# Kernel tuning notes

Hardware: AMD Instinct MI355X
Metric: run time of the kernel (lower is better)

## Reference

```python
import jax, jax.numpy as jnp
import numpy as np

N_NODES = 50000
N_EDGES = 1000000
IN_F = 128
OUT_F = 32
HEADS = 4


def setup_inputs() -> dict:
    key = jax.random.key(0)
    k1, k2, k3, k4, k5 = jax.random.split(key, 5)
    x = jax.random.normal(k1, (N_NODES, IN_F), dtype=jnp.float32)
    edge_index = jax.random.randint(k2, (2, N_EDGES), 0, N_NODES, dtype=jnp.int64)
    # nn.Linear weight: [out_features*heads, in_features], xavier_uniform
    lim_W = float(np.sqrt(6.0 / (IN_F + OUT_F * HEADS)))
    W = jax.random.uniform(k3, (OUT_F * HEADS, IN_F), dtype=jnp.float32, minval=-lim_W, maxval=lim_W)
    lim_a = float(np.sqrt(6.0 / (HEADS + OUT_F)))  # xavier on [1, heads, out]
    a_src = jax.random.uniform(k4, (1, HEADS, OUT_F), dtype=jnp.float32, minval=-lim_a, maxval=lim_a)
    a_dst = jax.random.uniform(k5, (1, HEADS, OUT_F), dtype=jnp.float32, minval=-lim_a, maxval=lim_a)
    return {"x": x, "edge_index": edge_index, "W": W, "a_src": a_src, "a_dst": a_dst}


def reference(x, edge_index, W, a_src, a_dst):
    N = x.shape[0]
    h, f = HEADS, OUT_F
    # Linear (no bias) then split heads: [N, h, f]
    x_trans = (x @ W.T).reshape(N, h, f)
    src, dst = edge_index[0], edge_index[1]
    x_src = x_trans[src]                      # [E, h, f] edge gather
    x_dst = x_trans[dst]                      # [E, h, f]
    attn_src = jnp.einsum('ehf,ohf->eh', x_src, a_src)  # a_* have leading 1 broadcast dim
    attn_dst = jnp.einsum('ehf,ohf->eh', x_dst, a_dst)
    scores = jax.nn.leaky_relu(attn_src + attn_dst, negative_slope=0.2)  # [E, h]
    # Faithful to original: softmax over dim=0 (ALL edges globally per head)
    attn_w = jax.nn.softmax(scores, axis=0)   # [E, h]; dropout = identity (eval)
    weighted = x_src * attn_w[:, :, None]     # [E, h, f]
    out = jax.ops.segment_sum(weighted, dst, num_segments=N)  # scatter-add over dst
    return out.reshape(N, h * f)
```

## Files before the change

### kernel.cpp

```cpp
#include <hip/hip_runtime.h>

#define HEADS 4
#define BKSH 5
#define CAP 896
#define MAXBK 1600

typedef short bf16x8 __attribute__((ext_vector_type(8)));
typedef float f32x4  __attribute__((ext_vector_type(4)));

__device__ __forceinline__ unsigned short f2bf(float f) {
    unsigned u = __float_as_uint(f);
    return (unsigned short)((u + 0x7FFFu + ((u >> 16) & 1u)) >> 16);
}
__device__ __forceinline__ int detect64(const int* __restrict__ ei32) {
    unsigned long long b = __ballot(ei32[2 * (threadIdx.x & 63) + 1] != 0);
    return (b == 0ULL) ? 1 : 0;
}
__device__ __forceinline__ void load_edge(const void* ei, int is64, long E, long e,
                                          long* s, long* d) {
    if (is64) {
        *s = (long)((const long long*)ei)[e];
        *d = (long)((const long long*)ei)[E + e];
    } else {
        *s = (long)((const int*)ei)[e];
        *d = (long)((const int*)ei)[E + e];
    }
}

__launch_bounds__(256)
__global__ void k_prep(const float* __restrict__ W, const float* __restrict__ avs,
                       const float* __restrict__ avd, unsigned short* __restrict__ Wb,
                       float* __restrict__ gs, float* __restrict__ gd,
                       int* __restrict__ cursor, float* __restrict__ sums, int nbk) {
    const int b = blockIdx.x, t = threadIdx.x;
    if (b < 16) {
        const int i = (b * 256 + t) * 4;
        const float4 v = *(const float4*)(W + i);
        ushort4 u;
        u.x = f2bf(v.x); u.y = f2bf(v.y); u.z = f2bf(v.z); u.w = f2bf(v.w);
        *(ushort4*)(Wb + i) = u;
    } else if (b == 16) {
        const int h = t >> 6, k0 = (t & 63) * 2;
        float s0 = 0.f, s1 = 0.f, d0 = 0.f, d1 = 0.f;
        for (int o = 0; o < 32; ++o) {
            const float as = avs[h * 32 + o], ad = avd[h * 32 + o];
            const float w0 = W[(h * 32 + o) * 128 + k0];
            const float w1 = W[(h * 32 + o) * 128 + k0 + 1];
            s0 = fmaf(as, w0, s0); s1 = fmaf(as, w1, s1);
            d0 = fmaf(ad, w0, d0); d1 = fmaf(ad, w1, d1);
        }
        gs[h * 128 + k0] = s0; gs[h * 128 + k0 + 1] = s1;
        gd[h * 128 + k0] = d0; gd[h * 128 + k0 + 1] = d1;
    } else {
        for (int i = t; i < nbk; i += 256) cursor[i] = 0;
        if (t < 4) sums[t] = 0.f;
    }
}

__launch_bounds__(256)
__global__ void k_mfma_scores(const float* __restrict__ x, const unsigned short* __restrict__ Wb,
                              const float* __restrict__ gs, const float* __restrict__ gd,
                              unsigned short* __restrict__ xt, float* __restrict__ ss,
                              float* __restrict__ sd, int N, int NG) {
    if ((int)blockIdx.x >= NG) {
        const int lane = threadIdx.x & 63;
        const int wid = __builtin_amdgcn_readfirstlane(threadIdx.x >> 6);
        const int n = ((int)blockIdx.x - NG) * 64 + lane;
        if (n >= N) return;
        const float4* __restrict__ xr  = (const float4*)(x + (long)n * 128);
        const float4* __restrict__ gsr = (const float4*)(gs + wid * 128);
        const float4* __restrict__ gdr = (const float4*)(gd + wid * 128);
        float vs = 0.f, vd = 0.f;
#pragma unroll
        for (int j = 0; j < 32; ++j) {
            const float4 xv = xr[j];
            const float4 gv = gsr[j];
            const float4 dv = gdr[j];
            vs = fmaf(xv.x, gv.x, fmaf(xv.y, gv.y, fmaf(xv.z, gv.z, fmaf(xv.w, gv.w, vs))));
            vd = fmaf(xv.x, dv.x, fmaf(xv.y, dv.y, fmaf(xv.z, dv.z, fmaf(xv.w, dv.w, vd))));
        }
        ss[n * 4 + wid] = vs;
        sd[n * 4 + wid] = vd;
        return;
    }
    const int lane = threadIdx.x & 63;
    const int wid = threadIdx.x >> 6;
    const int c = lane & 15, g = lane >> 4;
    const int m0 = blockIdx.x * 64 + wid * 16;
    const long row = (long)((m0 + c) < N ? (m0 + c) : (N - 1));
    const float4* __restrict__ xr = (const float4*)(x + row * 128);

    bf16x8 A[4];
#pragma unroll
    for (int ks = 0; ks < 4; ++ks) {
        const float4 f0 = xr[ks * 8 + g * 2];
        const float4 f1 = xr[ks * 8 + g * 2 + 1];
        bf16x8 a;
        a[0] = (short)f2bf(f0.x); a[1] = (short)f2bf(f0.y);
        a[2] = (short)f2bf(f0.z); a[3] = (short)f2bf(f0.w);
        a[4] = (short)f2bf(f1.x); a[5] = (short)f2bf(f1.y);
        a[6] = (short)f2bf(f1.z); a[7] = (short)f2bf(f1.w);
        A[ks] = a;
    }
#pragma unroll
    for (int to = 0; to < 8; ++to) {
        f32x4 acc = {0.f, 0.f, 0.f, 0.f};
#pragma unroll
        for (int ks = 0; ks < 4; ++ks) {
            const bf16x8 bv = *(const bf16x8*)(Wb + (long)(to * 16 + c) * 128 + ks * 32 + g * 8);
            acc = __builtin_amdgcn_mfma_f32_16x16x32_bf16(A[ks], bv, acc, 0, 0, 0);
        }
#pragma unroll
        for (int j = 0; j < 4; ++j) {
            const int n = m0 + g * 4 + j;
            if (n < N) xt[(long)n * 128 + to * 16 + c] = f2bf(acc[j]);
        }
    }
}

__launch_bounds__(1024)
__global__ void k_part(const void* __restrict__ ei, const float* __restrict__ ss,
                       const float* __restrict__ sd, int* __restrict__ cursor,
                       unsigned* __restrict__ ebuf, float* __restrict__ sums,
                       long E, int nbk) {
    __shared__ int hist[MAXBK];
    __shared__ int base[MAXBK];
    __shared__ float sm[16][4];
    const int t = threadIdx.x;
    const int is64 = detect64((const int*)ei);
    for (int i = t; i < nbk; i += 1024) hist[i] = 0;
    __syncthreads();

    const long e0 = (long)blockIdx.x * 4096;
    int sreg[4], dreg[4], rreg[4];
    float w0 = 0.f, w1 = 0.f, w2 = 0.f, w3 = 0.f;
#pragma unroll
    for (int j = 0; j < 4; ++j) {
        const long e = e0 + (long)j * 1024 + t;
        sreg[j] = -1;
        if (e < E) {
            long s, d;
            load_edge(ei, is64, E, e, &s, &d);
            sreg[j] = (int)s; dreg[j] = (int)d;
            rreg[j] = atomicAdd(&hist[(int)d >> BKSH], 1);
            const float4 a = ((const float4*)ss)[s];
            const float4 b = ((const float4*)sd)[d];
            float sc;
            sc = a.x + b.x; sc = sc > 0.f ? sc : 0.2f * sc; w0 += __expf(sc);
            sc = a.y + b.y; sc = sc > 0.f ? sc : 0.2f * sc; w1 += __expf(sc);
            sc = a.z + b.z; sc = sc > 0.f ? sc : 0.2f * sc; w2 += __expf(sc);
            sc = a.w + b.w; sc = sc > 0.f ? sc : 0.2f * sc; w3 += __expf(sc);
        }
    }
    __syncthreads();
    for (int i = t; i < nbk; i += 1024)
        base[i] = hist[i] ? atomicAdd(&cursor[i], hist[i]) : 0;
    __syncthreads();
#pragma unroll
    for (int j = 0; j < 4; ++j) {
        if (sreg[j] >= 0) {
            const int b = dreg[j] >> BKSH;
            const int pos = base[b] + rreg[j];
            if (pos < CAP)
                ebuf[(long)b * CAP + pos] =
                    ((unsigned)(dreg[j] & 31) << 16) | (unsigned)sreg[j];
        }
    }
#pragma unroll
    for (int m = 32; m; m >>= 1) {
        w0 += __shfl_xor(w0, m);
        w1 += __shfl_xor(w1, m);
        w2 += __shfl_xor(w2, m);
        w3 += __shfl_xor(w3, m);
    }
    const int wvi = t >> 6;
    if ((t & 63) == 0) { sm[wvi][0] = w0; sm[wvi][1] = w1; sm[wvi][2] = w2; sm[wvi][3] = w3; }
    __syncthreads();
    if (t < 4) {
        float v = 0.f;
#pragma unroll
        for (int i = 0; i < 16; ++i) v += sm[i][t];
        atomicAdd(&sums[t], v);
    }
}

__launch_bounds__(256)
__global__ void k_bgather(const unsigned* __restrict__ ebuf, const int* __restrict__ cursor,
                          const float* __restrict__ ss, const float* __restrict__ sd,
                          const float* __restrict__ sums, const unsigned* __restrict__ xt16,
                          float* __restrict__ out, int N) {
    __shared__ int cnt[32];
    __shared__ int row[33];
    __shared__ int cur[32];
    __shared__ unsigned lsrc[CAP];
    __shared__ float4 lwt[CAP];
    const int t = threadIdx.x;
    const int b = blockIdx.x;
    const int n0 = b << BKSH;
    if (t < 32) cnt[t] = 0;
    __syncthreads();
    const int c0v = cursor[b];
    const int m = c0v < CAP ? c0v : CAP;
    const unsigned* __restrict__ seg = ebuf + (long)b * CAP;
    for (int i = t; i < m; i += 256) atomicAdd(&cnt[seg[i] >> 16], 1);
    __syncthreads();
    if (t < 32) {
        const int v = cnt[t];
        int incl = v;
#pragma unroll
        for (int s = 1; s < 32; s <<= 1) {
            const int u = __shfl_up(incl, s);
            if (t >= s) incl += u;
        }
        row[t] = incl - v;
        cur[t] = incl - v;
        if (t == 31) row[32] = incl;
    }
    __syncthreads();
    for (int i = t; i < m; i += 256) {
        const unsigned u = seg[i];
        const int s = (int)(u & 0xFFFFu), dl = (int)(u >> 16);
        const int pos = atomicAdd(&cur[dl], 1);
        lsrc[pos] = (unsigned)s;
        const float4 a = ((const float4*)ss)[s];
        const float4 bb = ((const float4*)sd)[n0 + dl];
        float4 w; float sc;
        sc = a.x + bb.x; sc = sc > 0.f ? sc : 0.2f * sc; w.x = __expf(sc);
        sc = a.y + bb.y; sc = sc > 0.f ? sc : 0.2f * sc; w.y = __expf(sc);
        sc = a.z + bb.z; sc = sc > 0.f ? sc : 0.2f * sc; w.z = __expf(sc);
        sc = a.w + bb.w; sc = sc > 0.f ? sc : 0.2f * sc; w.w = __expf(sc);
        lwt[pos] = w;
    }
    __syncthreads();

    const int wv = t >> 6, l = t & 63, h = l >> 4;
    const float* __restrict__ lwtf = (const float*)lwt;
    const float invh = 1.0f / sums[h];
    for (int d8 = 0; d8 < 8; ++d8) {
        const int dl = wv * 8 + d8;
        const int n = n0 + dl;
        if (n >= N) break;
        const int beg = row[dl], end = row[dl + 1];
        float ax = 0.f, ay = 0.f;
        int i = beg;
        for (; i + 4 <= end; i += 4) {
            const int s0 = (int)lsrc[i + 0];
            const int s1 = (int)lsrc[i + 1];
            const int s2 = (int)lsrc[i + 2];
            const int s3 = (int)lsrc[i + 3];
            const float w0 = lwtf[(i + 0) * 4 + h];
            const float w1 = lwtf[(i + 1) * 4 + h];
            const float w2 = lwtf[(i + 2) * 4 + h];
            const float w3 = lwtf[(i + 3) * 4 + h];
            const unsigned x0 = xt16[(long)s0 * 64 + l];
            const unsigned x1 = xt16[(long)s1 * 64 + l];
            const unsigned x2 = xt16[(long)s2 * 64 + l];
            const unsigned x3 = xt16[(long)s3 * 64 + l];
            ax = fmaf(w0, __uint_as_float(x0 << 16), ax);
            ay = fmaf(w0, __uint_as_float(x0 & 0xFFFF0000u), ay);
            ax = fmaf(w1, __uint_as_float(x1 << 16), ax);
            ay = fmaf(w1, __uint_as_float(x1 & 0xFFFF0000u), ay);
            ax = fmaf(w2, __uint_as_float(x2 << 16), ax);
            ay = fmaf(w2, __uint_as_float(x2 & 0xFFFF0000u), ay);
            ax = fmaf(w3, __uint_as_float(x3 << 16), ax);
            ay = fmaf(w3, __uint_as_float(x3 & 0xFFFF0000u), ay);
        }
        for (; i < end; ++i) {
            const int s = (int)lsrc[i];
            const float wt = lwtf[i * 4 + h];
            const unsigned xv = xt16[(long)s * 64 + l];
            ax = fmaf(wt, __uint_as_float(xv << 16), ax);
            ay = fmaf(wt, __uint_as_float(xv & 0xFFFF0000u), ay);
        }
        ((float2*)out)[(long)n * 64 + l] = make_float2(ax * invh, ay * invh);
    }
}

extern "C" void kernel_launch(void* const* d_in, const int* in_sizes, int n_in,
                              void* d_out, int out_size, void* d_ws, size_t ws_size,
                              hipStream_t stream) {
    const float* x     = (const float*)d_in[0];
    const void*  ei    = d_in[1];
    const float* W     = (const float*)d_in[2];
    const float* a_src = (const float*)d_in[3];
    const float* a_dst = (const float*)d_in[4];
    const long N = in_sizes[0] / 128;
    const long E = in_sizes[1] / 2;
    const int NG  = (int)((N + 63) / 64);
    const int nbk = (int)((N + 31) / 32);
    const int NP  = (int)((E + 4095) / 4096);

    char* p = (char*)d_ws;
    auto alloc = [&](size_t bytes) { char* r = p; p += (bytes + 15) & ~(size_t)15; return r; };
    unsigned*       xt16   = (unsigned*)alloc(N * 64 * 4);
    float*          ss     = (float*)alloc(N * 4 * 4);
    float*          sd     = (float*)alloc(N * 4 * 4);
    unsigned*       ebuf   = (unsigned*)alloc((size_t)nbk * CAP * 4);
    int*            cursor = (int*)alloc(nbk * 4);
    float*          sums   = (float*)alloc(4 * 4);
    unsigned short* Wb     = (unsigned short*)alloc(128 * 128 * 2);
    float*          gs     = (float*)alloc(4 * 128 * 4);
    float*          gd     = (float*)alloc(4 * 128 * 4);

    float* out = (float*)d_out;

    k_prep<<<18, 256, 0, stream>>>(W, a_src, a_dst, Wb, gs, gd, cursor, sums, nbk);
    k_mfma_scores<<<(unsigned)(2 * NG), 256, 0, stream>>>(x, Wb, gs, gd,
                                                          (unsigned short*)xt16,
                                                          ss, sd, (int)N, NG);
    k_part<<<(unsigned)NP, 1024, 0, stream>>>(ei, ss, sd, cursor, ebuf, sums, E, nbk);
    k_bgather<<<(unsigned)nbk, 256, 0, stream>>>(ebuf, cursor, ss, sd, sums, xt16,
                                                 out, (int)N);
}
```

Baseline: 105.1 us.

## Fuse attention score projection into MFMA linear kernel; unroll gather by eight

The src/dst score dot products (x·gs, x·gd) move into the MFMA transform kernel. They reuse the x rows each lane already loads for the bf16 A fragments, with partial sums reduced across the four lane groups by shuffles. This drops the separate half of the grid that re-read all of x in fp32, halving x traffic in that stage. The gather loop in k_bgather is also unrolled from 4 to 8 edges so more independent loads are in flight, at some cost in register pressure.

```diff
diff --git a/kernel.cpp b/kernel.cpp
--- a/kernel.cpp
+++ b/kernel.cpp
@@ -58,39 +58,29 @@
 }
 
 __launch_bounds__(256)
-__global__ void k_mfma_scores(const float* __restrict__ x, const unsigned short* __restrict__ Wb,
-                              const float* __restrict__ gs, const float* __restrict__ gd,
-                              unsigned short* __restrict__ xt, float* __restrict__ ss,
-                              float* __restrict__ sd, int N, int NG) {
-    if ((int)blockIdx.x >= NG) {
-        const int lane = threadIdx.x & 63;
-        const int wid = __builtin_amdgcn_readfirstlane(threadIdx.x >> 6);
-        const int n = ((int)blockIdx.x - NG) * 64 + lane;
-        if (n >= N) return;
-        const float4* __restrict__ xr  = (const float4*)(x + (long)n * 128);
-        const float4* __restrict__ gsr = (const float4*)(gs + wid * 128);
-        const float4* __restrict__ gdr = (const float4*)(gd + wid * 128);
-        float vs = 0.f, vd = 0.f;
-#pragma unroll
-        for (int j = 0; j < 32; ++j) {
-            const float4 xv = xr[j];
-            const float4 gv = gsr[j];
-            const float4 dv = gdr[j];
-            vs = fmaf(xv.x, gv.x, fmaf(xv.y, gv.y, fmaf(xv.z, gv.z, fmaf(xv.w, gv.w, vs))));
-            vd = fmaf(xv.x, dv.x, fmaf(xv.y, dv.y, fmaf(xv.z, dv.z, fmaf(xv.w, dv.w, vd))));
-        }
-        ss[n * 4 + wid] = vs;
-        sd[n * 4 + wid] = vd;
-        return;
-    }
-    const int lane = threadIdx.x & 63;
-    const int wid = threadIdx.x >> 6;
+__global__ void k_mfma(const float* __restrict__ x, const unsigned short* __restrict__ Wb,
+                       const float* __restrict__ gs, const float* __restrict__ gd,
+                       unsigned short* __restrict__ xt, float* __restrict__ ss,
+                       float* __restrict__ sd, int N) {
+    __shared__ float gsl[512], gdl[512];
+    const int t = threadIdx.x;
+    if (t < 128) {
+        ((float4*)gsl)[t] = ((const float4*)gs)[t];
+        ((float4*)gdl)[t] = ((const float4*)gd)[t];
+    }
+    __syncthreads();
+
+    const int lane = t & 63;
+    const int wid = t >> 6;
     const int c = lane & 15, g = lane >> 4;
     const int m0 = blockIdx.x * 64 + wid * 16;
-    const long row = (long)((m0 + c) < N ? (m0 + c) : (N - 1));
+    const int nrow = m0 + c;
+    const long row = (long)(nrow < N ? nrow : (N - 1));
     const float4* __restrict__ xr = (const float4*)(x + row * 128);
 
     bf16x8 A[4];
+    float vs0 = 0.f, vs1 = 0.f, vs2 = 0.f, vs3 = 0.f;
+    float vd0 = 0.f, vd1 = 0.f, vd2 = 0.f, vd3 = 0.f;
 #pragma unroll
     for (int ks = 0; ks < 4; ++ks) {
         const float4 f0 = xr[ks * 8 + g * 2];
@@ -101,7 +91,36 @@
         a[4] = (short)f2bf(f1.x); a[5] = (short)f2bf(f1.y);
         a[6] = (short)f2bf(f1.z); a[7] = (short)f2bf(f1.w);
         A[ks] = a;
-    }
+        const int kb = ks * 32 + g * 8;
+#pragma unroll
+        for (int h = 0; h < 4; ++h) {
+            const float4 G0 = *(const float4*)(gsl + h * 128 + kb);
+            const float4 G1 = *(const float4*)(gsl + h * 128 + kb + 4);
+            const float4 D0 = *(const float4*)(gdl + h * 128 + kb);
+            const float4 D1 = *(const float4*)(gdl + h * 128 + kb + 4);
+            float s = fmaf(f0.x, G0.x, fmaf(f0.y, G0.y, fmaf(f0.z, G0.z, f0.w * G0.w)));
+            s = fmaf(f1.x, G1.x, fmaf(f1.y, G1.y, fmaf(f1.z, G1.z, fmaf(f1.w, G1.w, s))));
+            float d = fmaf(f0.x, D0.x, fmaf(f0.y, D0.y, fmaf(f0.z, D0.z, f0.w * D0.w)));
+            d = fmaf(f1.x, D1.x, fmaf(f1.y, D1.y, fmaf(f1.z, D1.z, fmaf(f1.w, D1.w, d))));
+            if (h == 0) { vs0 += s; vd0 += d; }
+            else if (h == 1) { vs1 += s; vd1 += d; }
+            else if (h == 2) { vs2 += s; vd2 += d; }
+            else { vs3 += s; vd3 += d; }
+        }
+    }
+    vs0 += __shfl_xor(vs0, 16); vs0 += __shfl_xor(vs0, 32);
+    vs1 += __shfl_xor(vs1, 16); vs1 += __shfl_xor(vs1, 32);
+    vs2 += __shfl_xor(vs2, 16); vs2 += __shfl_xor(vs2, 32);
+    vs3 += __shfl_xor(vs3, 16); vs3 += __shfl_xor(vs3, 32);
+    vd0 += __shfl_xor(vd0, 16); vd0 += __shfl_xor(vd0, 32);
+    vd1 += __shfl_xor(vd1, 16); vd1 += __shfl_xor(vd1, 32);
+    vd2 += __shfl_xor(vd2, 16); vd2 += __shfl_xor(vd2, 32);
+    vd3 += __shfl_xor(vd3, 16); vd3 += __shfl_xor(vd3, 32);
+    if (g == 0 && nrow < N) {
+        ((float4*)ss)[nrow] = make_float4(vs0, vs1, vs2, vs3);
+        ((float4*)sd)[nrow] = make_float4(vd0, vd1, vd2, vd3);
+    }
+
 #pragma unroll
     for (int to = 0; to < 8; ++to) {
         f32x4 acc = {0.f, 0.f, 0.f, 0.f};
@@ -243,27 +262,19 @@
         const int beg = row[dl], end = row[dl + 1];
         float ax = 0.f, ay = 0.f;
         int i = beg;
-        for (; i + 4 <= end; i += 4) {
-            const int s0 = (int)lsrc[i + 0];
-            const int s1 = (int)lsrc[i + 1];
-            const int s2 = (int)lsrc[i + 2];
-            const int s3 = (int)lsrc[i + 3];
-            const float w0 = lwtf[(i + 0) * 4 + h];
-            const float w1 = lwtf[(i + 1) * 4 + h];
-            const float w2 = lwtf[(i + 2) * 4 + h];
-            const float w3 = lwtf[(i + 3) * 4 + h];
-            const unsigned x0 = xt16[(long)s0 * 64 + l];
-            const unsigned x1 = xt16[(long)s1 * 64 + l];
-            const unsigned x2 = xt16[(long)s2 * 64 + l];
-            const unsigned x3 = xt16[(long)s3 * 64 + l];
-            ax = fmaf(w0, __uint_as_float(x0 << 16), ax);
-            ay = fmaf(w0, __uint_as_float(x0 & 0xFFFF0000u), ay);
-            ax = fmaf(w1, __uint_as_float(x1 << 16), ax);
-            ay = fmaf(w1, __uint_as_float(x1 & 0xFFFF0000u), ay);
-            ax = fmaf(w2, __uint_as_float(x2 << 16), ax);
-            ay = fmaf(w2, __uint_as_float(x2 & 0xFFFF0000u), ay);
-            ax = fmaf(w3, __uint_as_float(x3 << 16), ax);
-            ay = fmaf(w3, __uint_as_float(x3 & 0xFFFF0000u), ay);
+        for (; i + 8 <= end; i += 8) {
+            int sarr[8]; float warr[8]; unsigned xv[8];
+#pragma unroll
+            for (int j = 0; j < 8; ++j) sarr[j] = (int)lsrc[i + j];
+#pragma unroll
+            for (int j = 0; j < 8; ++j) warr[j] = lwtf[(i + j) * 4 + h];
+#pragma unroll
+            for (int j = 0; j < 8; ++j) xv[j] = xt16[(long)sarr[j] * 64 + l];
+#pragma unroll
+            for (int j = 0; j < 8; ++j) {
+                ax = fmaf(warr[j], __uint_as_float(xv[j] << 16), ax);
+                ay = fmaf(warr[j], __uint_as_float(xv[j] & 0xFFFF0000u), ay);
+            }
         }
         for (; i < end; ++i) {
             const int s = (int)lsrc[i];
@@ -304,10 +315,9 @@
 
     float* out = (float*)d_out;
 
-    k_prep<<<18, 256, 0, stream>>>(W, a_src, a_dst, Wb, gs, gd, cursor, sums, nbk);
-    k_mfma_scores<<<(unsigned)(2 * NG), 256, 0, stream>>>(x, Wb, gs, gd,
-                                                          (unsigned short*)xt16,
-                                                          ss, sd, (int)N, NG);
+    k_prep<<<18, 256, 0, stream>>>(W, a_src, a_dst, Wb, gs, gd, cursor, sums, (int)nbk);
+    k_mfma<<<(unsigned)NG, 256, 0, stream>>>(x, Wb, gs, gd, (unsigned short*)xt16,
+                                             ss, sd, (int)N);
     k_part<<<(unsigned)NP, 1024, 0, stream>>>(ei, ss, sd, cursor, ebuf, sums, E, nbk);
     k_bgather<<<(unsigned)nbk, 256, 0, stream>>>(ebuf, cursor, ss, sd, sums, xt16,
                                                  out, (int)N);
```

Measured after the change: 97.74 us. -7.0%, faster.

## Reschedule kernels: fold scores into prep, run MFMA projection alongside edge partition

Applied to the files above, without the earlier changes.

The pipeline is regrouped from four launches into three. The per-node attention-score dot products now run in the prep kernel, with the folded attention vectors recomputed per block into shared memory. The bf16 MFMA projection now shares one launch with the edge partition/histogram pass at 512 threads per block. This removes a launch boundary and lets the GEMM and the edge bucketing overlap on the GPU. The cost is that every score block redundantly recomputes the gs/gd vectors, and the partition blocks change shape (512 threads, 8 edges per thread).

```diff
diff --git a/kernel.cpp b/kernel.cpp
--- a/kernel.cpp
+++ b/kernel.cpp
@@ -28,10 +28,11 @@
 }
 
 __launch_bounds__(256)
-__global__ void k_prep(const float* __restrict__ W, const float* __restrict__ avs,
-                       const float* __restrict__ avd, unsigned short* __restrict__ Wb,
-                       float* __restrict__ gs, float* __restrict__ gd,
-                       int* __restrict__ cursor, float* __restrict__ sums, int nbk) {
+__global__ void k_pre(const float* __restrict__ W, const float* __restrict__ avs,
+                      const float* __restrict__ avd, const float* __restrict__ x,
+                      unsigned short* __restrict__ Wb, float* __restrict__ ss,
+                      float* __restrict__ sd, int* __restrict__ cursor,
+                      float* __restrict__ sums, int nbk, int N) {
     const int b = blockIdx.x, t = threadIdx.x;
     if (b < 16) {
         const int i = (b * 256 + t) * 4;
@@ -39,7 +40,15 @@
         ushort4 u;
         u.x = f2bf(v.x); u.y = f2bf(v.y); u.z = f2bf(v.z); u.w = f2bf(v.w);
         *(ushort4*)(Wb + i) = u;
-    } else if (b == 16) {
+        return;
+    }
+    if (b == 16) {
+        for (int i = t; i < nbk; i += 256) cursor[i] = 0;
+        if (t < 4) sums[t] = 0.f;
+        return;
+    }
+    __shared__ float gsl[512], gdl[512];
+    {
         const int h = t >> 6, k0 = (t & 63) * 2;
         float s0 = 0.f, s1 = 0.f, d0 = 0.f, d1 = 0.f;
         for (int o = 0; o < 32; ++o) {
@@ -49,94 +58,87 @@
             s0 = fmaf(as, w0, s0); s1 = fmaf(as, w1, s1);
             d0 = fmaf(ad, w0, d0); d1 = fmaf(ad, w1, d1);
         }
-        gs[h * 128 + k0] = s0; gs[h * 128 + k0 + 1] = s1;
-        gd[h * 128 + k0] = d0; gd[h * 128 + k0 + 1] = d1;
-    } else {
-        for (int i = t; i < nbk; i += 256) cursor[i] = 0;
-        if (t < 4) sums[t] = 0.f;
-    }
-}
-
-__launch_bounds__(256)
-__global__ void k_mfma_scores(const float* __restrict__ x, const unsigned short* __restrict__ Wb,
-                              const float* __restrict__ gs, const float* __restrict__ gd,
-                              unsigned short* __restrict__ xt, float* __restrict__ ss,
-                              float* __restrict__ sd, int N, int NG) {
-    if ((int)blockIdx.x >= NG) {
-        const int lane = threadIdx.x & 63;
-        const int wid = __builtin_amdgcn_readfirstlane(threadIdx.x >> 6);
-        const int n = ((int)blockIdx.x - NG) * 64 + lane;
-        if (n >= N) return;
-        const float4* __restrict__ xr  = (const float4*)(x + (long)n * 128);
-        const float4* __restrict__ gsr = (const float4*)(gs + wid * 128);
-        const float4* __restrict__ gdr = (const float4*)(gd + wid * 128);
-        float vs = 0.f, vd = 0.f;
-#pragma unroll
-        for (int j = 0; j < 32; ++j) {
-            const float4 xv = xr[j];
-            const float4 gv = gsr[j];
-            const float4 dv = gdr[j];
-            vs = fmaf(xv.x, gv.x, fmaf(xv.y, gv.y, fmaf(xv.z, gv.z, fmaf(xv.w, gv.w, vs))));
-            vd = fmaf(xv.x, dv.x, fmaf(xv.y, dv.y, fmaf(xv.z, dv.z, fmaf(xv.w, dv.w, vd))));
-        }
-        ss[n * 4 + wid] = vs;
-        sd[n * 4 + wid] = vd;
-        return;
-    }
-    const int lane = threadIdx.x & 63;
-    const int wid = threadIdx.x >> 6;
-    const int c = lane & 15, g = lane >> 4;
-    const int m0 = blockIdx.x * 64 + wid * 16;
-    const long row = (long)((m0 + c) < N ? (m0 + c) : (N - 1));
-    const float4* __restrict__ xr = (const float4*)(x + row * 128);
-
-    bf16x8 A[4];
-#pragma unroll
-    for (int ks = 0; ks < 4; ++ks) {
-        const float4 f0 = xr[ks * 8 + g * 2];
-        const float4 f1 = xr[ks * 8 + g * 2 + 1];
-        bf16x8 a;
-        a[0] = (short)f2bf(f0.x); a[1] = (short)f2bf(f0.y);
-        a[2] = (short)f2bf(f0.z); a[3] = (short)f2bf(f0.w);
-        a[4] = (short)f2bf(f1.x); a[5] = (short)f2bf(f1.y);
-        a[6] = (short)f2bf(f1.z); a[7] = (short)f2bf(f1.w);
-        A[ks] = a;
-    }
-#pragma unroll
-    for (int to = 0; to < 8; ++to) {
-        f32x4 acc = {0.f, 0.f, 0.f, 0.f};
-#pragma unroll
-        for (int ks = 0; ks < 4; ++ks) {
-            const bf16x8 bv = *(const bf16x8*)(Wb + (long)(to * 16 + c) * 128 + ks * 32 + g * 8);
-            acc = __builtin_amdgcn_mfma_f32_16x16x32_bf16(A[ks], bv, acc, 0, 0, 0);
-        }
-#pragma unroll
-        for (int j = 0; j < 4; ++j) {
-            const int n = m0 + g * 4 + j;
-            if (n < N) xt[(long)n * 128 + to * 16 + c] = f2bf(acc[j]);
-        }
-    }
-}
-
-__launch_bounds__(1024)
-__global__ void k_part(const void* __restrict__ ei, const float* __restrict__ ss,
-                       const float* __restrict__ sd, int* __restrict__ cursor,
-                       unsigned* __restrict__ ebuf, float* __restrict__ sums,
-                       long E, int nbk) {
+        gsl[h * 128 + k0] = s0; gsl[h * 128 + k0 + 1] = s1;
+        gdl[h * 128 + k0] = d0; gdl[h * 128 + k0 + 1] = d1;
+    }
+    __syncthreads();
+    const int lane = t & 63;
+    const int wid = t >> 6;
+    const int n = (b - 17) * 64 + lane;
+    if (n >= N) return;
+    const float4* __restrict__ xr  = (const float4*)(x + (long)n * 128);
+    const float4* __restrict__ gsr = (const float4*)(gsl + wid * 128);
+    const float4* __restrict__ gdr = (const float4*)(gdl + wid * 128);
+    float vs = 0.f, vd = 0.f;
+#pragma unroll
+    for (int j = 0; j < 32; ++j) {
+        const float4 xv = xr[j];
+        const float4 gv = gsr[j];
+        const float4 dv = gdr[j];
+        vs = fmaf(xv.x, gv.x, fmaf(xv.y, gv.y, fmaf(xv.z, gv.z, fmaf(xv.w, gv.w, vs))));
+        vd = fmaf(xv.x, dv.x, fmaf(xv.y, dv.y, fmaf(xv.z, dv.z, fmaf(xv.w, dv.w, vd))));
+    }
+    ss[n * 4 + wid] = vs;
+    sd[n * 4 + wid] = vd;
+}
+
+__launch_bounds__(512)
+__global__ void k_mp(const float* __restrict__ x, const unsigned short* __restrict__ Wb,
+                     const void* __restrict__ ei, const float* __restrict__ ss,
+                     const float* __restrict__ sd, unsigned short* __restrict__ xt,
+                     int* __restrict__ cursor, unsigned* __restrict__ ebuf,
+                     float* __restrict__ sums, int N, int NG2, long E, int nbk) {
     __shared__ int hist[MAXBK];
     __shared__ int base[MAXBK];
-    __shared__ float sm[16][4];
+    __shared__ float sm[8][4];
     const int t = threadIdx.x;
+    if ((int)blockIdx.x < NG2) {
+        const int lane = t & 63;
+        const int wid = t >> 6;
+        const int c = lane & 15, g = lane >> 4;
+        const int m0 = blockIdx.x * 128 + wid * 16;
+        const int nrow = m0 + c;
+        const long row = (long)(nrow < N ? nrow : (N - 1));
+        const float4* __restrict__ xr = (const float4*)(x + row * 128);
+
+        bf16x8 A[4];
+#pragma unroll
+        for (int ks = 0; ks < 4; ++ks) {
+            const float4 f0 = xr[ks * 8 + g * 2];
+            const float4 f1 = xr[ks * 8 + g * 2 + 1];
+            bf16x8 a;
+            a[0] = (short)f2bf(f0.x); a[1] = (short)f2bf(f0.y);
+            a[2] = (short)f2bf(f0.z); a[3] = (short)f2bf(f0.w);
+            a[4] = (short)f2bf(f1.x); a[5] = (short)f2bf(f1.y);
+            a[6] = (short)f2bf(f1.z); a[7] = (short)f2bf(f1.w);
+            A[ks] = a;
+        }
+#pragma unroll
+        for (int to = 0; to < 8; ++to) {
+            f32x4 acc = {0.f, 0.f, 0.f, 0.f};
+#pragma unroll
+            for (int ks = 0; ks < 4; ++ks) {
+                const bf16x8 bv = *(const bf16x8*)(Wb + (long)(to * 16 + c) * 128 + ks * 32 + g * 8);
+                acc = __builtin_amdgcn_mfma_f32_16x16x32_bf16(A[ks], bv, acc, 0, 0, 0);
+            }
+#pragma unroll
+            for (int j = 0; j < 4; ++j) {
+                const int n = m0 + g * 4 + j;
+                if (n < N) xt[(long)n * 128 + to * 16 + c] = f2bf(acc[j]);
+            }
+        }
+        return;
+    }
     const int is64 = detect64((const int*)ei);
-    for (int i = t; i < nbk; i += 1024) hist[i] = 0;
-    __syncthreads();
-
-    const long e0 = (long)blockIdx.x * 4096;
-    int sreg[4], dreg[4], rreg[4];
+    for (int i = t; i < nbk; i += 512) hist[i] = 0;
+    __syncthreads();
+
+    const long e0 = (long)((int)blockIdx.x - NG2) * 4096;
+    int sreg[8], dreg[8], rreg[8];
     float w0 = 0.f, w1 = 0.f, w2 = 0.f, w3 = 0.f;
 #pragma unroll
-    for (int j = 0; j < 4; ++j) {
-        const long e = e0 + (long)j * 1024 + t;
+    for (int j = 0; j < 8; ++j) {
+        const long e = e0 + (long)j * 512 + t;
         sreg[j] = -1;
         if (e < E) {
             long s, d;
@@ -153,11 +155,11 @@
         }
     }
     __syncthreads();
-    for (int i = t; i < nbk; i += 1024)
+    for (int i = t; i < nbk; i += 512)
         base[i] = hist[i] ? atomicAdd(&cursor[i], hist[i]) : 0;
     __syncthreads();
 #pragma unroll
-    for (int j = 0; j < 4; ++j) {
+    for (int j = 0; j < 8; ++j) {
         if (sreg[j] >= 0) {
             const int b = dreg[j] >> BKSH;
             const int pos = base[b] + rreg[j];
@@ -179,7 +181,7 @@
     if (t < 4) {
         float v = 0.f;
 #pragma unroll
-        for (int i = 0; i < 16; ++i) v += sm[i][t];
+        for (int i = 0; i < 8; ++i) v += sm[i][t];
         atomicAdd(&sums[t], v);
     }
 }
@@ -287,6 +289,7 @@
     const long N = in_sizes[0] / 128;
     const long E = in_sizes[1] / 2;
     const int NG  = (int)((N + 63) / 64);
+    const int NG2 = (int)((N + 127) / 128);
     const int nbk = (int)((N + 31) / 32);
     const int NP  = (int)((E + 4095) / 4096);
 
@@ -299,16 +302,14 @@
     int*            cursor = (int*)alloc(nbk * 4);
     float*          sums   = (float*)alloc(4 * 4);
     unsigned short* Wb     = (unsigned short*)alloc(128 * 128 * 2);
-    float*          gs     = (float*)alloc(4 * 128 * 4);
-    float*          gd     = (float*)alloc(4 * 128 * 4);
 
     float* out = (float*)d_out;
 
-    k_prep<<<18, 256, 0, stream>>>(W, a_src, a_dst, Wb, gs, gd, cursor, sums, nbk);
-    k_mfma_scores<<<(unsigned)(2 * NG), 256, 0, stream>>>(x, Wb, gs, gd,
-                                                          (unsigned short*)xt16,
-                                                          ss, sd, (int)N, NG);
-    k_part<<<(unsigned)NP, 1024, 0, stream>>>(ei, ss, sd, cursor, ebuf, sums, E, nbk);
+    k_pre<<<(unsigned)(17 + NG), 256, 0, stream>>>(W, a_src, a_dst, x, Wb, ss, sd,
+                                                   cursor, sums, nbk, (int)N);
+    k_mp<<<(unsigned)(NG2 + NP), 512, 0, stream>>>(x, Wb, ei, ss, sd,
+                                                   (unsigned short*)xt16, cursor,
+                                                   ebuf, sums, (int)N, NG2, E, nbk);
     k_bgather<<<(unsigned)nbk, 256, 0, stream>>>(ebuf, cursor, ss, sd, sums, xt16,
                                                  out, (int)N);
 }
```

Result: faster. 99.88 us (-5.0%).
